# Kernel optimization log

Measured on AMD Instinct MI355X. Metric: run time of the kernel, lower is better.

## Reference

```python
import math
import jax, jax.numpy as jnp
import numpy as np

N, L, C_IMG, D, FF, H, NL, V = 2, 1024, 512, 512, 2048, 8, 4, 8000
EPS_ATTN = 1e-6
EPS_LN = 1e-5


def pos_enc(position, channels):
    # position: (N, L, 1) float. channels assumed even here (256 / 512).
    num = channels // 2
    log_inc = math.log(10000.0) / (num - 1)
    inv = jnp.exp(jnp.arange(num, dtype=position.dtype) * -log_inc)
    st = position * inv.reshape(1, 1, -1)  # (N, L, num)
    return jnp.concatenate([jnp.sin(st), jnp.cos(st)], -1)


def layer_norm(x, s, b):
    m = jnp.mean(x, -1, keepdims=True)
    v = jnp.mean((x - m) ** 2, -1, keepdims=True)
    return (x - m) / jnp.sqrt(v + EPS_LN) * s + b


def causal_linear_attention(x, mask, Wq, bq, Wk, bk, Wv, bv, Wo, bo):
    # x: (N, L, D), mask: (N, L, 1)
    n, l, d = x.shape
    q = (x @ Wq + bq).reshape(n, l, H, -1)
    k = (x @ Wk + bk).reshape(n, l, H, -1)
    v = (x @ Wv + bv).reshape(n, l, H, -1)
    Q = jax.nn.elu(q) + 1.0                       # elu feature map
    K = (jax.nn.elu(k) + 1.0) * mask[:, :, :, None]
    K_cum = jnp.cumsum(K, axis=1)                 # (N, L, H, dk)
    Z = 1.0 / (jnp.einsum('nlhd,nlhd->nlh', Q, K_cum) + EPS_ATTN)
    KV = jnp.cumsum(K[..., :, None] * v[..., None, :], axis=1)  # (N, L, H, dk, dv)
    out = jnp.einsum('nlhd,nlhde->nlhe', Q, KV) * Z[..., None]
    return out.reshape(n, l, d) @ Wo + bo


def encoder_layer(x, mask, p):
    (Wq, bq, Wk, bk, Wv, bv, Wo, bo, W1, b1, W2, b2, s1, be1, s2, be2) = p
    x = x + causal_linear_attention(x, mask, Wq, bq, Wk, bk, Wv, bv, Wo, bo)
    x = layer_norm(x, s1, be1)
    y = jax.nn.gelu(x @ W1 + b1, approximate=False) @ W2 + b2
    return layer_norm(x + y, s2, be2)


def setup_inputs() -> dict:
    key = jax.random.key(0)
    ks = iter(jax.random.split(key, 64))

    def p(shape):
        return jax.random.normal(next(ks), shape, dtype=jnp.float32) * 0.02

    x_img = jax.random.normal(next(ks), (N, L, C_IMG), dtype=jnp.float32)
    x_txt = jax.random.randint(next(ks), (N, L), 0, V)
    pos = jnp.broadcast_to(jnp.arange(L, dtype=jnp.float32)[None, :, None], (N, L, 1))
    pos_r = jnp.floor(pos / 32.0)
    pos_c = jnp.mod(pos, 32.0)
    pos_t = pos
    first_half = (jnp.arange(L) < L // 2).astype(jnp.float32)[None, :, None]
    mask_img = jnp.broadcast_to(first_half, (N, L, 1))
    mask_txt = 1.0 - mask_img

    inp = dict(x_img=x_img, x_txt=x_txt, mask_img=mask_img, mask_txt=mask_txt,
               pos_r=pos_r, pos_c=pos_c, pos_t=pos_t,
               W_ei=p((C_IMG, D)), b_ei=jnp.zeros((D,)),
               emb_txt=p((V, D)),
               Wq=p((NL, D, D)), bq=jnp.zeros((NL, D)),
               Wk=p((NL, D, D)), bk=jnp.zeros((NL, D)),
               Wv=p((NL, D, D)), bv=jnp.zeros((NL, D)),
               Wo=p((NL, D, D)), bo=jnp.zeros((NL, D)),
               W1=p((NL, D, FF)), b1=jnp.zeros((NL, FF)),
               W2=p((NL, FF, D)), b2=jnp.zeros((NL, D)),
               ln1_s=jnp.ones((NL, D)), ln1_b=jnp.zeros((NL, D)),
               ln2_s=jnp.ones((NL, D)), ln2_b=jnp.zeros((NL, D)),
               W_pi=p((D, C_IMG)), b_pi=jnp.zeros((C_IMG,)),
               W_pt=p((D, V)), b_pt=jnp.zeros((V,)))
    return inp


def reference(x_img, x_txt, mask_img, mask_txt, pos_r, pos_c, pos_t,
              W_ei, b_ei, emb_txt,
              Wq, bq, Wk, bk, Wv, bv, Wo, bo, W1, b1, W2, b2,
              ln1_s, ln1_b, ln2_s, ln2_b, W_pi, b_pi, W_pt, b_pt):
    x_mask = mask_img + mask_txt  # (N, L, 1)
    # image embedding
    half = D // 2
    x_pos = jnp.concatenate([pos_enc(pos_r, half), pos_enc(pos_c, D - half)], -1)
    x_emb_img = ((x_img @ W_ei + b_ei) + x_pos) * mask_img
    # text embedding
    x_emb_txt = (emb_txt[x_txt] + pos_enc(pos_t, D)) * mask_txt
    x = x_emb_img + x_emb_txt
    for i in range(NL):
        p = (Wq[i], bq[i], Wk[i], bk[i], Wv[i], bv[i], Wo[i], bo[i],
             W1[i], b1[i], W2[i], b2[i], ln1_s[i], ln1_b[i], ln2_s[i], ln2_b[i])
        x = encoder_layer(x, x_mask, p)
    logit_img = x @ W_pi + b_pi
    logit_txt = x @ W_pt + b_pt
    return (logit_img, logit_txt)
```

## Files before the change

### kernel.cpp

```cpp
#include <hip/hip_runtime.h>
#include <hip/hip_bf16.h>
#include <math.h>

#define NB 2
#define LSEQ 1024
#define DM 512
#define FFD 2048
#define NHEAD 8
#define DKH 64
#define NLAYER 4
#define VOCAB 8000
#define NCHUNK 16
#define NROWS (NB * LSEQ)
#define QS 1536
#define NHEADCAT 8512
#define NHEADPAD 8576

#define OP_NONE 0
#define OP_GELU 2
#define OP_QKV  3
#define OP_PART 4
#define OP_HEAD 5

typedef __attribute__((ext_vector_type(8))) short short8;
typedef __attribute__((ext_vector_type(4))) float f32x4;
typedef __hip_bfloat16 bf16;

__device__ __forceinline__ void cast_tile(
    const float* __restrict__ s, bf16* __restrict__ d, int K, int N,
    int n0, int k0, int tx, int ty)
{
    __shared__ float tile[32][33];
    #pragma unroll
    for (int i = 0; i < 4; ++i) {
        const int k = k0 + ty + 8 * i;
        const int n = n0 + tx;
        tile[ty + 8 * i][tx] = (n < N) ? s[(size_t)k * N + n] : 0.f;
    }
    __syncthreads();
    #pragma unroll
    for (int i = 0; i < 4; ++i) {
        const int n = n0 + ty + 8 * i;
        d[(size_t)n * K + k0 + tx] = __float2bfloat16(tile[tx][ty + 8 * i]);
    }
}

#define CO_QKVO 0
#define CO_W1   4096
#define CO_W2   8192
#define CO_WEI  12288
#define CO_WPI  12544
#define CO_WPT  12800
#define CO_XIMG 16832
#define CO_QKVB 17856
#define CO_HB   17860
#define CO_END  17894

__global__ __launch_bounds__(256) void setup_all(
    const float* __restrict__ Wq, const float* __restrict__ Wk,
    const float* __restrict__ Wv, const float* __restrict__ Wo,
    const float* __restrict__ W1, const float* __restrict__ W2,
    const float* __restrict__ Wei, const float* __restrict__ Wpi,
    const float* __restrict__ Wpt,
    bf16* __restrict__ QKVt, bf16* __restrict__ Wot,
    bf16* __restrict__ W1t, bf16* __restrict__ W2t,
    bf16* __restrict__ Weit, bf16* __restrict__ Whead,
    const float* __restrict__ x_img, bf16* __restrict__ ximgh,
    const float* __restrict__ bq, const float* __restrict__ bk,
    const float* __restrict__ bv, float* __restrict__ qkvB,
    const float* __restrict__ bpi, const float* __restrict__ bpt,
    float* __restrict__ hb)
{
    const int id = blockIdx.x;
    const int tid = threadIdx.x;
    const int tx = tid & 31, ty = tid >> 5;

    if (id < CO_W1) {
        const int rel = id;
        const int z = rel >> 8, t = rel & 255;
        const int layer = z >> 2, which = z & 3;
        const float* src = (which == 0 ? Wq : which == 1 ? Wk : which == 2 ? Wv : Wo)
                           + (size_t)layer * 262144;
        bf16* dst = (which < 3)
            ? (QKVt + (size_t)layer * 786432 + (size_t)which * 262144)
            : (Wot + (size_t)layer * 262144);
        cast_tile(src, dst, 512, 512, (t & 15) * 32, (t >> 4) * 32, tx, ty);
    } else if (id < CO_W2) {
        const int rel = id - CO_W1;
        const int z = rel >> 10, t = rel & 1023;
        cast_tile(W1 + (size_t)z * 1048576, W1t + (size_t)z * 1048576,
                  512, 2048, (t & 63) * 32, (t >> 6) * 32, tx, ty);
    } else if (id < CO_WEI) {
        const int rel = id - CO_W2;
        const int z = rel >> 10, t = rel & 1023;
        cast_tile(W2 + (size_t)z * 1048576, W2t + (size_t)z * 1048576,
                  2048, 512, (t & 15) * 32, (t >> 4) * 32, tx, ty);
    } else if (id < CO_WPI) {
        const int t = id - CO_WEI;
        cast_tile(Wei, Weit, 512, 512, (t & 15) * 32, (t >> 4) * 32, tx, ty);
    } else if (id < CO_WPT) {
        const int t = id - CO_WPI;
        cast_tile(Wpi, Whead, 512, 512, (t & 15) * 32, (t >> 4) * 32, tx, ty);
    } else if (id < CO_XIMG) {
        const int t = id - CO_WPT;
        cast_tile(Wpt, Whead + 262144, 512, VOCAB,
                  (t % 252) * 32, (t / 252) * 32, tx, ty);
    } else if (id < CO_QKVB) {
        const int i = (id - CO_XIMG) * 256 + tid;
        const float4 v = *(const float4*)(x_img + (size_t)i * 4);
        ximgh[(size_t)i * 4 + 0] = __float2bfloat16(v.x);
        ximgh[(size_t)i * 4 + 1] = __float2bfloat16(v.y);
        ximgh[(size_t)i * 4 + 2] = __float2bfloat16(v.z);
        ximgh[(size_t)i * 4 + 3] = __float2bfloat16(v.w);
    } else if (id < CO_HB) {
        const int z = id - CO_QKVB;
        for (int j = tid; j < QS; j += 256) {
            float v;
            if (j < 512)       v = bq[z * DM + j];
            else if (j < 1024) v = bk[z * DM + j - 512];
            else               v = bv[z * DM + j - 1024];
            qkvB[z * QS + j] = v;
        }
    } else {
        const int j = (id - CO_HB) * 256 + tid;
        if (j < NHEADPAD)
            hb[j] = (j < 512) ? bpi[j] : (j < NHEADCAT ? bpt[j - 512] : 0.f);
    }
}

template<int BM, int BN>
__global__ __launch_bounds__(256) void gemm16(
    const bf16* __restrict__ A, const bf16* __restrict__ Bt,
    const float* __restrict__ bias, const float* __restrict__ res,
    float* __restrict__ outF, float* __restrict__ outF2,
    bf16* __restrict__ outH,
    int M, int K, int Nout, int op, int kslab)
{
    constexpr int WM = BM / 2, WN = BN / 2, MI = WM / 16, NI = WN / 16;
    __shared__ bf16 As[BM * 32];
    __shared__ bf16 Bs[BN * 32];
    const int tid = threadIdx.x;
    const int lane = tid & 63;
    const int wave = tid >> 6;
    const int wm = (wave >> 1) * WM, wn = (wave & 1) * WN;

    int bxi = blockIdx.x, byi = blockIdx.y;
    if (op == OP_HEAD) {
        const int gx = gridDim.x;
        const int nwg = gx * gridDim.y;
        int flat = byi * gx + bxi;
        const int q = nwg >> 3, r = nwg & 7;
        const int xcd = flat & 7, lid = flat >> 3;
        flat = (xcd < r ? xcd * (q + 1) : r * (q + 1) + (xcd - r) * q) + lid;
        bxi = flat % gx;
        byi = flat / gx;
    }
    const int bm = (op == OP_HEAD ? bxi : blockIdx.y) * BM;
    const int bn = (op == OP_HEAD ? byi : blockIdx.x) * BN;
    const int l16 = lane & 15, quad = lane >> 4;

    const int rA = tid >> 2;
    const int c8 = (tid & 3) << 3;

    f32x4 acc[MI][NI];
    #pragma unroll
    for (int i = 0; i < MI; ++i)
        #pragma unroll
        for (int j = 0; j < NI; ++j) acc[i][j] = (f32x4){0.f, 0.f, 0.f, 0.f};

    const bf16* gA = A  + (size_t)(bm + rA) * K + c8;
    const bf16* gB = Bt + (size_t)(bn + rA) * K + c8;
    const int ldsWaveOff = wave * 1024;

    const int kStart = blockIdx.z * kslab;
    for (int k0 = kStart; k0 < kStart + kslab; k0 += 32) {
        __syncthreads();
        #pragma unroll
        for (int i = 0; i < BM / 64; ++i)
            __builtin_amdgcn_global_load_lds(
                (const __attribute__((address_space(1))) void*)(gA + (size_t)i * 64 * K + k0),
                (__attribute__((address_space(3))) void*)((char*)As + i * 4096 + ldsWaveOff),
                16, 0, 0);
        #pragma unroll
        for (int i = 0; i < BN / 64; ++i)
            __builtin_amdgcn_global_load_lds(
                (const __attribute__((address_space(1))) void*)(gB + (size_t)i * 64 * K + k0),
                (__attribute__((address_space(3))) void*)((char*)Bs + i * 4096 + ldsWaveOff),
                16, 0, 0);
        __syncthreads();
        short8 a[MI], b[NI];
        #pragma unroll
        for (int i = 0; i < MI; ++i)
            a[i] = *(const short8*)(As + (size_t)(wm + i * 16 + l16) * 32 + quad * 8);
        #pragma unroll
        for (int j = 0; j < NI; ++j)
            b[j] = *(const short8*)(Bs + (size_t)(wn + j * 16 + l16) * 32 + quad * 8);
        #pragma unroll
        for (int i = 0; i < MI; ++i)
            #pragma unroll
            for (int j = 0; j < NI; ++j)
                acc[i][j] = __builtin_amdgcn_mfma_f32_16x16x32_bf16(
                    a[i], b[j], acc[i][j], 0, 0, 0);
    }

    if (op == OP_PART) {
        float* dst = outF + (size_t)blockIdx.z * (size_t)M * Nout;
        #pragma unroll
        for (int j = 0; j < NI; ++j) {
            const int col = bn + wn + j * 16 + l16;
            #pragma unroll
            for (int i = 0; i < MI; ++i)
                #pragma unroll
                for (int r = 0; r < 4; ++r) {
                    const int row = bm + wm + i * 16 + quad * 4 + r;
                    dst[(size_t)row * Nout + col] = acc[i][j][r];
                }
        }
        return;
    }
    if (op == OP_HEAD) {
        #pragma unroll
        for (int j = 0; j < NI; ++j) {
            const int col = bn + wn + j * 16 + l16;
            const bool cok = (col < NHEADCAT);
            const float bz = cok ? bias[col] : 0.f;
            #pragma unroll
            for (int i = 0; i < MI; ++i)
                #pragma unroll
                for (int r = 0; r < 4; ++r) {
                    const int row = bm + wm + i * 16 + quad * 4 + r;
                    const float v = acc[i][j][r] + bz;
                    if (cok) {
                        if (col < 512) outF[(size_t)row * 512 + col] = v;
                        else           outF2[(size_t)row * VOCAB + (col - 512)] = v;
                    }
                }
        }
        return;
    }

    #pragma unroll
    for (int j = 0; j < NI; ++j) {
        const int col = bn + wn + j * 16 + l16;
        const bool cok = (col < Nout);
        const float bz = cok ? bias[col] : 0.f;
        #pragma unroll
        for (int i = 0; i < MI; ++i) {
            #pragma unroll
            for (int r = 0; r < 4; ++r) {
                const int row = bm + wm + i * 16 + quad * 4 + r;
                float v = acc[i][j][r] + bz;
                if (op == OP_GELU)      v = 0.5f * v * (1.f + erff(v * 0.70710678118654752f));
                else if (op == OP_QKV && col < 1024) v = (v > 0.f) ? v + 1.f : expf(v);
                if (cok) {
                    if (res)  v += res[(size_t)row * Nout + col];
                    if (outF) outF[(size_t)row * Nout + col] = v;
                    if (outH) outH[(size_t)row * Nout + col] = __float2bfloat16(v);
                }
            }
        }
    }
}

__global__ __launch_bounds__(256) void embed_k(
    const float* __restrict__ gI, const int* __restrict__ xt,
    const float* __restrict__ emb,
    const float* __restrict__ mi, const float* __restrict__ mt,
    const float* __restrict__ pr, const float* __restrict__ pc,
    const float* __restrict__ pt, float* __restrict__ X, bf16* __restrict__ Xh)
{
    const int row = blockIdx.x;
    const float prv = pr[row], pcv = pc[row], ptv = pt[row];
    const float miv = mi[row], mtv = mt[row];
    const int tok = xt[row];
    const float LOG1E4 = 9.2103403719761836f;
    const float LI127 = LOG1E4 / 127.f;
    const float LI255 = LOG1E4 / 255.f;

    for (int d = threadIdx.x; d < DM; d += 256) {
        float ip;
        if (d < 128)       ip = sinf(prv * expf(-(float)d * LI127));
        else if (d < 256)  ip = cosf(prv * expf(-(float)(d - 128) * LI127));
        else if (d < 384)  ip = sinf(pcv * expf(-(float)(d - 256) * LI127));
        else               ip = cosf(pcv * expf(-(float)(d - 384) * LI127));
        float tp;
        if (d < 256) tp = sinf(ptv * expf(-(float)d * LI255));
        else         tp = cosf(ptv * expf(-(float)(d - 256) * LI255));
        const float v = miv * (gI[(size_t)row * DM + d] + ip)
                      + mtv * (emb[(size_t)tok * DM + d] + tp);
        X[(size_t)row * DM + d] = v;
        Xh[(size_t)row * DM + d] = __float2bfloat16(v);
    }
}

__global__ __launch_bounds__(256) void ln_red(
    const float* __restrict__ P, int nP,
    const float* __restrict__ bias, const float* __restrict__ res,
    const float* __restrict__ g, const float* __restrict__ b,
    float* __restrict__ out, bf16* __restrict__ outh)
{
    const int row = blockIdx.x;
    const int tid = threadIdx.x;
    const int lane = tid & 63, wv = tid >> 6;
    const size_t base = (size_t)row * DM;
    float x0 = res[base + tid] + bias[tid];
    float x1 = res[base + tid + 256] + bias[tid + 256];
    for (int p = 0; p < nP; ++p) {
        x0 += P[(size_t)p * 1048576 + base + tid];
        x1 += P[(size_t)p * 1048576 + base + tid + 256];
    }
    __shared__ float redA[4];
    __shared__ float redB[4];
    float s = x0 + x1;
    #pragma unroll
    for (int off = 32; off > 0; off >>= 1) s += __shfl_down(s, off);
    if (lane == 0) redA[wv] = s;
    __syncthreads();
    const float mean = (redA[0] + redA[1] + redA[2] + redA[3]) * (1.f / (float)DM);
    const float d0 = x0 - mean, d1 = x1 - mean;
    float v = d0 * d0 + d1 * d1;
    #pragma unroll
    for (int off = 32; off > 0; off >>= 1) v += __shfl_down(v, off);
    if (lane == 0) redB[wv] = v;
    __syncthreads();
    const float var = (redB[0] + redB[1] + redB[2] + redB[3]) * (1.f / (float)DM);
    const float rstd = rsqrtf(var + 1e-5f);
    const float y0 = d0 * rstd * g[tid] + b[tid];
    const float y1 = d1 * rstd * g[tid + 256] + b[tid + 256];
    out[base + tid]        = y0;
    out[base + tid + 256]  = y1;
    outh[base + tid]       = __float2bfloat16(y0);
    outh[base + tid + 256] = __float2bfloat16(y1);
}

__global__ __launch_bounds__(256) void attn_kv(
    const float* __restrict__ Kp, const float* __restrict__ Vp,
    float* __restrict__ S, float* __restrict__ ks)
{
    const int c = blockIdx.x, h = blockIdx.y, n = blockIdx.z;
    const int tid = threadIdx.x;
    __shared__ float sK[64][64], sV[64][64], part[4][64];

    const int lr = tid >> 4;
    const int c4 = (tid & 15) * 4;
    #pragma unroll
    for (int it = 0; it < 4; ++it) {
        const int row = it * 16 + lr;
        const size_t gb = ((size_t)(n * LSEQ + c * 64 + row)) * QS + h * DKH + c4;
        *(float4*)&sK[row][c4] = *(const float4*)(Kp + gb);
        *(float4*)&sV[row][c4] = *(const float4*)(Vp + gb);
    }
    __syncthreads();

    const int e = tid & 63, dq = tid >> 6;
    float s[16] = {};
    for (int l = 0; l < 64; ++l) {
        const float vv = sV[l][e];
        const float4 k0 = *(const float4*)&sK[l][dq * 16 + 0];
        const float4 k1 = *(const float4*)&sK[l][dq * 16 + 4];
        const float4 k2 = *(const float4*)&sK[l][dq * 16 + 8];
        const float4 k3 = *(const float4*)&sK[l][dq * 16 + 12];
        s[0]  = fmaf(k0.x, vv, s[0]);  s[1]  = fmaf(k0.y, vv, s[1]);
        s[2]  = fmaf(k0.z, vv, s[2]);  s[3]  = fmaf(k0.w, vv, s[3]);
        s[4]  = fmaf(k1.x, vv, s[4]);  s[5]  = fmaf(k1.y, vv, s[5]);
        s[6]  = fmaf(k1.z, vv, s[6]);  s[7]  = fmaf(k1.w, vv, s[7]);
        s[8]  = fmaf(k2.x, vv, s[8]);  s[9]  = fmaf(k2.y, vv, s[9]);
        s[10] = fmaf(k2.z, vv, s[10]); s[11] = fmaf(k2.w, vv, s[11]);
        s[12] = fmaf(k3.x, vv, s[12]); s[13] = fmaf(k3.y, vv, s[13]);
        s[14] = fmaf(k3.z, vv, s[14]); s[15] = fmaf(k3.w, vv, s[15]);
    }
    const size_t sb = (((size_t)(n * NHEAD + h)) * NCHUNK + c) * 4096;
    #pragma unroll
    for (int i = 0; i < 16; ++i) S[sb + (size_t)(dq * 16 + i) * 64 + e] = s[i];

    float kp = 0.f;
    #pragma unroll
    for (int i = 0; i < 16; ++i) kp += sK[dq * 16 + i][e];
    part[dq][e] = kp;
    __syncthreads();
    if (tid < 64)
        ks[(((size_t)(n * NHEAD + h)) * NCHUNK + c) * 64 + tid] =
            part[0][tid] + part[1][tid] + part[2][tid] + part[3][tid];
}

__global__ __launch_bounds__(256) void attn_out(
    const float* __restrict__ QKV, const float* __restrict__ S,
    const float* __restrict__ ks, bf16* __restrict__ O)
{
    const int c = blockIdx.x, h = blockIdx.y, n = blockIdx.z;
    const int tid = threadIdx.x;
    __shared__ float sQt[64][64];
    __shared__ float sKt[64][64];
    __shared__ float sV [64][64];
    __shared__ float sS [64][64];
    __shared__ float sPt[64][65];
    __shared__ float skp[64];

    const size_t nhS = ((size_t)(n * NHEAD + h)) * NCHUNK * 4096;
    const size_t nhK = ((size_t)(n * NHEAD + h)) * NCHUNK * 64;

    {
        float4 aS[4] = {};
        for (int cc = 0; cc < c; ++cc) {
            const float* Sc = S + nhS + (size_t)cc * 4096;
            #pragma unroll
            for (int i = 0; i < 4; ++i) {
                const float4 t = *(const float4*)(Sc + i * 1024 + tid * 4);
                aS[i].x += t.x; aS[i].y += t.y; aS[i].z += t.z; aS[i].w += t.w;
            }
        }
        float* sSf = &sS[0][0];
        #pragma unroll
        for (int i = 0; i < 4; ++i)
            *(float4*)(sSf + i * 1024 + tid * 4) = aS[i];
        if (tid < 64) {
            float kp = 0.f;
            for (int cc = 0; cc < c; ++cc) kp += ks[nhK + cc * 64 + tid];
            skp[tid] = kp;
        }
    }

    const int lr = tid >> 4;
    const int c4 = (tid & 15) * 4;
    #pragma unroll
    for (int it = 0; it < 4; ++it) {
        const int row = it * 16 + lr;
        const size_t gb = ((size_t)(n * LSEQ + c * 64 + row)) * QS + h * DKH + c4;
        const float4 q4 = *(const float4*)(QKV + gb);
        const float4 k4 = *(const float4*)(QKV + gb + 512);
        const float4 v4 = *(const float4*)(QKV + gb + 1024);
        sQt[c4 + 0][row] = q4.x; sQt[c4 + 1][row] = q4.y;
        sQt[c4 + 2][row] = q4.z; sQt[c4 + 3][row] = q4.w;
        sKt[c4 + 0][row] = k4.x; sKt[c4 + 1][row] = k4.y;
        sKt[c4 + 2][row] = k4.z; sKt[c4 + 3][row] = k4.w;
        *(float4*)&sV[row][c4] = v4;
    }
    __syncthreads();

    const int m4 = (tid & 15) * 4;
    const int lg = tid >> 4;
    {
        float p[4][4] = {};
        for (int d = 0; d < 64; ++d) {
            const float4 k4 = *(const float4*)&sKt[d][m4];
            const float4 q4 = *(const float4*)&sQt[d][lg * 4];
            p[0][0] = fmaf(q4.x, k4.x, p[0][0]); p[0][1] = fmaf(q4.x, k4.y, p[0][1]);
            p[0][2] = fmaf(q4.x, k4.z, p[0][2]); p[0][3] = fmaf(q4.x, k4.w, p[0][3]);
            p[1][0] = fmaf(q4.y, k4.x, p[1][0]); p[1][1] = fmaf(q4.y, k4.y, p[1][1]);
            p[1][2] = fmaf(q4.y, k4.z, p[1][2]); p[1][3] = fmaf(q4.y, k4.w, p[1][3]);
            p[2][0] = fmaf(q4.z, k4.x, p[2][0]); p[2][1] = fmaf(q4.z, k4.y, p[2][1]);
            p[2][2] = fmaf(q4.z, k4.z, p[2][2]); p[2][3] = fmaf(q4.z, k4.w, p[2][3]);
            p[3][0] = fmaf(q4.w, k4.x, p[3][0]); p[3][1] = fmaf(q4.w, k4.y, p[3][1]);
            p[3][2] = fmaf(q4.w, k4.z, p[3][2]); p[3][3] = fmaf(q4.w, k4.w, p[3][3]);
        }
        #pragma unroll
        for (int jj = 0; jj < 4; ++jj)
            #pragma unroll
            for (int j = 0; j < 4; ++j)
                sPt[m4 + jj][lg * 4 + j] = p[j][jj];
    }
    __syncthreads();

    float acc[4][4] = {};
    float z[4] = {};
    const int lmax = lg * 4 + 3;
    for (int m = 0; m <= lmax; ++m) {
        const float4 v4 = *(const float4*)&sV[m][m4];
        #pragma unroll
        for (int j = 0; j < 4; ++j) {
            const int l = lg * 4 + j;
            float p = sPt[m][l];
            p = (m <= l) ? p : 0.f;
            z[j] += p;
            acc[j][0] = fmaf(p, v4.x, acc[j][0]);
            acc[j][1] = fmaf(p, v4.y, acc[j][1]);
            acc[j][2] = fmaf(p, v4.z, acc[j][2]);
            acc[j][3] = fmaf(p, v4.w, acc[j][3]);
        }
    }
    for (int d = 0; d < 64; ++d) {
        const float4 s4 = *(const float4*)&sS[d][m4];
        const float4 q4 = *(const float4*)&sQt[d][lg * 4];
        const float kp = skp[d];
        z[0] = fmaf(q4.x, kp, z[0]); z[1] = fmaf(q4.y, kp, z[1]);
        z[2] = fmaf(q4.z, kp, z[2]); z[3] = fmaf(q4.w, kp, z[3]);
        acc[0][0] = fmaf(q4.x, s4.x, acc[0][0]); acc[0][1] = fmaf(q4.x, s4.y, acc[0][1]);
        acc[0][2] = fmaf(q4.x, s4.z, acc[0][2]); acc[0][3] = fmaf(q4.x, s4.w, acc[0][3]);
        acc[1][0] = fmaf(q4.y, s4.x, acc[1][0]); acc[1][1] = fmaf(q4.y, s4.y, acc[1][1]);
        acc[1][2] = fmaf(q4.y, s4.z, acc[1][2]); acc[1][3] = fmaf(q4.y, s4.w, acc[1][3]);
        acc[2][0] = fmaf(q4.z, s4.x, acc[2][0]); acc[2][1] = fmaf(q4.z, s4.y, acc[2][1]);
        acc[2][2] = fmaf(q4.z, s4.z, acc[2][2]); acc[2][3] = fmaf(q4.z, s4.w, acc[2][3]);
        acc[3][0] = fmaf(q4.w, s4.x, acc[3][0]); acc[3][1] = fmaf(q4.w, s4.y, acc[3][1]);
        acc[3][2] = fmaf(q4.w, s4.z, acc[3][2]); acc[3][3] = fmaf(q4.w, s4.w, acc[3][3]);
    }
    #pragma unroll
    for (int j = 0; j < 4; ++j) {
        const int l = lg * 4 + j;
        const float rz = 1.f / (z[j] + 1e-6f);
        const size_t ob = ((size_t)(n * LSEQ + c * 64 + l)) * DM + h * DKH + m4;
        O[ob + 0] = __float2bfloat16(acc[j][0] * rz);
        O[ob + 1] = __float2bfloat16(acc[j][1] * rz);
        O[ob + 2] = __float2bfloat16(acc[j][2] * rz);
        O[ob + 3] = __float2bfloat16(acc[j][3] * rz);
    }
}

extern "C" void kernel_launch(void* const* d_in, const int* in_sizes, int n_in,
                              void* d_out, int out_size, void* d_ws, size_t ws_size,
                              hipStream_t stream)
{
    const float* x_img   = (const float*)d_in[0];
    const int*   x_txt   = (const int*)  d_in[1];
    const float* mask_i  = (const float*)d_in[2];
    const float* mask_t  = (const float*)d_in[3];
    const float* pos_r   = (const float*)d_in[4];
    const float* pos_c   = (const float*)d_in[5];
    const float* pos_t   = (const float*)d_in[6];
    const float* W_ei    = (const float*)d_in[7];
    const float* b_ei    = (const float*)d_in[8];
    const float* emb_txt = (const float*)d_in[9];
    const float* Wq      = (const float*)d_in[10];
    const float* bq      = (const float*)d_in[11];
    const float* Wk      = (const float*)d_in[12];
    const float* bk      = (const float*)d_in[13];
    const float* Wv      = (const float*)d_in[14];
    const float* bv      = (const float*)d_in[15];
    const float* Wo      = (const float*)d_in[16];
    const float* bo      = (const float*)d_in[17];
    const float* W1      = (const float*)d_in[18];
    const float* b1      = (const float*)d_in[19];
    const float* W2      = (const float*)d_in[20];
    const float* b2      = (const float*)d_in[21];
    const float* ln1_s   = (const float*)d_in[22];
    const float* ln1_b   = (const float*)d_in[23];
    const float* ln2_s   = (const float*)d_in[24];
    const float* ln2_b   = (const float*)d_in[25];
    const float* W_pi    = (const float*)d_in[26];
    const float* b_pi    = (const float*)d_in[27];
    const float* W_pt    = (const float*)d_in[28];
    const float* b_pt    = (const float*)d_in[29];

    float* ws = (float*)d_ws;
    size_t off = 0;
    auto alloc = [&](size_t nfloats) { float* p = ws + off; off += nfloats; return p; };

    float* Xb   = alloc(1048576);
    float* Pb   = alloc(4194304);
    float* QKVb = alloc(3145728);
    float* Sb   = alloc(1048576);
    float* ksb  = alloc(16384);
    float* qkvB = alloc(4 * QS);
    float* hb   = alloc(8704);
    bf16* Xh    = (bf16*)alloc(524288);
    bf16* Ob    = (bf16*)alloc(524288);
    bf16* Tb    = (bf16*)alloc(2097152);
    bf16* ximgh = (bf16*)alloc(524288);
    bf16* QKVt  = (bf16*)alloc(1572864);
    bf16* Wot   = (bf16*)alloc(524288);
    bf16* W1t   = (bf16*)alloc(2097152);
    bf16* W2t   = (bf16*)alloc(2097152);
    bf16* Weit  = (bf16*)alloc(131072);
    bf16* Whead = (bf16*)alloc(2195456);

    const dim3 blk(256);
    const dim3 gAttn(NCHUNK, NHEAD, NB);

    setup_all<<<dim3(CO_END), blk, 0, stream>>>(
        Wq, Wk, Wv, Wo, W1, W2, W_ei, W_pi, W_pt,
        QKVt, Wot, W1t, W2t, Weit, Whead,
        x_img, ximgh, bq, bk, bv, qkvB, b_pi, b_pt, hb);

    gemm16<64, 64><<<dim3(8, 32), blk, 0, stream>>>(
        ximgh, Weit, b_ei, nullptr, Pb, nullptr, nullptr, NROWS, 512, 512, OP_NONE, 512);
    embed_k<<<NROWS, blk, 0, stream>>>(Pb, x_txt, emb_txt, mask_i, mask_t,
                                       pos_r, pos_c, pos_t, Xb, Xh);

    for (int i = 0; i < NLAYER; ++i) {
        gemm16<64, 128><<<dim3(12, 32), blk, 0, stream>>>(
            Xh, QKVt + (size_t)i * 786432, qkvB + i * QS, nullptr,
            QKVb, nullptr, nullptr, NROWS, 512, QS, OP_QKV, 512);

        attn_kv<<<gAttn, blk, 0, stream>>>(QKVb + 512, QKVb + 1024, Sb, ksb);
        attn_out<<<gAttn, blk, 0, stream>>>(QKVb, Sb, ksb, Ob);

        gemm16<64, 64><<<dim3(8, 32, 2), blk, 0, stream>>>(
            Ob, Wot + (size_t)i * 262144, nullptr, nullptr,
            Pb, nullptr, nullptr, NROWS, 512, 512, OP_PART, 256);
        ln_red<<<NROWS, blk, 0, stream>>>(Pb, 2, bo + (size_t)i * DM, Xb,
                                          ln1_s + (size_t)i * DM,
                                          ln1_b + (size_t)i * DM, Xb, Xh);

        gemm16<64, 128><<<dim3(16, 32), blk, 0, stream>>>(
            Xh, W1t + (size_t)i * 1048576, b1 + (size_t)i * FFD, nullptr,
            nullptr, nullptr, Tb, NROWS, 512, FFD, OP_GELU, 512);
        gemm16<64, 64><<<dim3(8, 32, 4), blk, 0, stream>>>(
            Tb, W2t + (size_t)i * 1048576, nullptr, nullptr,
            Pb, nullptr, nullptr, NROWS, 2048, 512, OP_PART, 512);
        ln_red<<<NROWS, blk, 0, stream>>>(Pb, 4, b2 + (size_t)i * DM, Xb,
                                          ln2_s + (size_t)i * DM,
                                          ln2_b + (size_t)i * DM, Xb, Xh);
    }

    float* out = (float*)d_out;
    gemm16<128, 128><<<dim3(16, 67), blk, 0, stream>>>(
        Xh, Whead, hb, nullptr, out, out + 1048576, nullptr,
        NROWS, 512, NHEADCAT, OP_HEAD, 512);
}
```

Before: 645.8 us.

## Double-buffer GEMM LDS tiles to overlap global loads with MFMA compute

The GEMM main loop now keeps two LDS buffers for the A and B tiles. It issues the async global-to-LDS loads for the next k-step before computing on the current one, using a partial vmcnt wait. This lets memory latency overlap with MFMA work instead of sitting between two full barriers. In exchange it doubles LDS usage, which can lower occupancy. It also relies on raw s_barrier and waitcnt ordering being correct.

```diff
diff --git a/kernel.cpp b/kernel.cpp
--- a/kernel.cpp
+++ b/kernel.cpp
@@ -137,8 +137,10 @@
     int M, int K, int Nout, int op, int kslab)
 {
     constexpr int WM = BM / 2, WN = BN / 2, MI = WM / 16, NI = WN / 16;
-    __shared__ bf16 As[BM * 32];
-    __shared__ bf16 Bs[BN * 32];
+    constexpr int LA = BM / 64, LB = BN / 64;
+    constexpr int NL = LA + LB;
+    __shared__ bf16 As[2][BM * 32];
+    __shared__ bf16 Bs[2][BN * 32];
     const int tid = threadIdx.x;
     const int lane = tid & 63;
     const int wave = tid >> 6;
@@ -173,34 +175,49 @@
     const int ldsWaveOff = wave * 1024;
 
     const int kStart = blockIdx.z * kslab;
-    for (int k0 = kStart; k0 < kStart + kslab; k0 += 32) {
-        __syncthreads();
-        #pragma unroll
-        for (int i = 0; i < BM / 64; ++i)
+    const int kEnd = kStart + kslab;
+
+    auto stage = [&](int buf, int k0) {
+        #pragma unroll
+        for (int i = 0; i < LA; ++i)
             __builtin_amdgcn_global_load_lds(
                 (const __attribute__((address_space(1))) void*)(gA + (size_t)i * 64 * K + k0),
-                (__attribute__((address_space(3))) void*)((char*)As + i * 4096 + ldsWaveOff),
+                (__attribute__((address_space(3))) void*)((char*)As[buf] + i * 4096 + ldsWaveOff),
                 16, 0, 0);
         #pragma unroll
-        for (int i = 0; i < BN / 64; ++i)
+        for (int i = 0; i < LB; ++i)
             __builtin_amdgcn_global_load_lds(
                 (const __attribute__((address_space(1))) void*)(gB + (size_t)i * 64 * K + k0),
-                (__attribute__((address_space(3))) void*)((char*)Bs + i * 4096 + ldsWaveOff),
+                (__attribute__((address_space(3))) void*)((char*)Bs[buf] + i * 4096 + ldsWaveOff),
                 16, 0, 0);
-        __syncthreads();
+    };
+
+    stage(0, kStart);
+    int cur = 0;
+    for (int k0 = kStart; k0 < kEnd; k0 += 32) {
+        const bool hasNext = (k0 + 32 < kEnd);
+        if (hasNext) {
+            stage(cur ^ 1, k0 + 32);
+            asm volatile("s_waitcnt vmcnt(%0)" :: "n"(NL) : "memory");
+        } else {
+            asm volatile("s_waitcnt vmcnt(0)" ::: "memory");
+        }
+        __builtin_amdgcn_s_barrier();
         short8 a[MI], b[NI];
         #pragma unroll
         for (int i = 0; i < MI; ++i)
-            a[i] = *(const short8*)(As + (size_t)(wm + i * 16 + l16) * 32 + quad * 8);
+            a[i] = *(const short8*)(As[cur] + (size_t)(wm + i * 16 + l16) * 32 + quad * 8);
         #pragma unroll
         for (int j = 0; j < NI; ++j)
-            b[j] = *(const short8*)(Bs + (size_t)(wn + j * 16 + l16) * 32 + quad * 8);
+            b[j] = *(const short8*)(Bs[cur] + (size_t)(wn + j * 16 + l16) * 32 + quad * 8);
         #pragma unroll
         for (int i = 0; i < MI; ++i)
             #pragma unroll
             for (int j = 0; j < NI; ++j)
                 acc[i][j] = __builtin_amdgcn_mfma_f32_16x16x32_bf16(
                     a[i], b[j], acc[i][j], 0, 0, 0);
+        __builtin_amdgcn_s_barrier();
+        cur ^= 1;
     }
 
     if (op == OP_PART) {
```

New measurement: 631.0 us. 1.02x faster.
